# Kernel optimization log

Measured on AMD Instinct MI355X. Metric: run time of the kernel, lower is better.

The kernel has to match this reference:

```python
import jax, jax.numpy as jnp
import numpy as np

B, S, D_IN = 4, 2048, 1024
EMBED, HEADS = 1024, 16
HEAD_DIM = EMBED // HEADS


def setup_inputs() -> dict:
    key = jax.random.key(0)
    k1, k2, k3 = jax.random.split(key, 3)
    x = jax.random.normal(k1, (B, S, D_IN), dtype=jnp.float32)
    # xavier-uniform-ish init scales
    lim_qkv = float(np.sqrt(6.0 / (D_IN + 3 * EMBED)))
    lim_o = float(np.sqrt(6.0 / (EMBED + EMBED)))
    w_qkv = jax.random.uniform(k2, (3 * EMBED, D_IN), minval=-lim_qkv, maxval=lim_qkv, dtype=jnp.float32)
    b_qkv = jnp.zeros((3 * EMBED,), dtype=jnp.float32)
    w_o = jax.random.uniform(k3, (EMBED, EMBED), minval=-lim_o, maxval=lim_o, dtype=jnp.float32)
    b_o = jnp.zeros((EMBED,), dtype=jnp.float32)
    return {"x": x, "w_qkv": w_qkv, "b_qkv": b_qkv, "w_o": w_o, "b_o": b_o}


def reference(x, w_qkv, b_qkv, w_o, b_o):
    b, s, _ = x.shape
    qkv = jnp.einsum('bsi,oi->bso', x, w_qkv) + b_qkv            # (b, s, 3E)
    qkv = qkv.reshape(b, s, HEADS, 3 * HEAD_DIM).transpose(0, 2, 1, 3)  # (b, h, s, 3d)
    q, k, v = jnp.split(qkv, 3, axis=-1)                          # each (b, h, s, d)
    scale = 1.0 / jnp.sqrt(jnp.float32(HEAD_DIM))
    attn = jnp.einsum('bhqd,bhkd->bhqk', q, k) * scale            # (b, h, s, s)
    attn = jax.nn.softmax(attn, axis=-1)
    vals = jnp.einsum('bhqk,bhkd->bhqd', attn, v)                 # (b, h, s, d)
    # NOTE: original torch code reshapes (b,h,s,d) -> (b,s,e) WITHOUT transposing
    # heads back; jnp.reshape reproduces that flattening exactly.
    vals = vals.reshape(b, s, EMBED)
    out = jnp.einsum('bse,oe->bso', vals, w_o) + b_o              # (b, s, E)
    return out
```

## Files before the change

### kernel.cpp

```cpp
#include <hip/hip_runtime.h>
#include <stdint.h>
#include <stddef.h>

#define DEVINL __device__ __forceinline__

typedef unsigned short u16;
typedef unsigned int u32;
typedef __attribute__((ext_vector_type(8))) short short8;
typedef __attribute__((ext_vector_type(4))) float f32x4;
typedef __attribute__((ext_vector_type(4))) u32 u32x4;
typedef __attribute__((ext_vector_type(2))) u32 u32x2;

#define QSCALE 0.18033688011112042f

DEVINL u16 f2bf(float f) {
    u32 u = __builtin_bit_cast(u32, f);
    u32 r = (u + 0x7fffu + ((u >> 16) & 1u)) >> 16;
    return (u16)r;
}

DEVINL void gld_lds16(const void* g, void* l) {
    __builtin_amdgcn_global_load_lds(
        (__attribute__((address_space(1))) u32*)(uintptr_t)g,
        (__attribute__((address_space(3))) u32*)l, 16, 0, 0);
}

DEVINL u32 pack_bf16_trunc(float lo, float hi) {
    return __builtin_amdgcn_perm(__builtin_bit_cast(u32, hi),
                                 __builtin_bit_cast(u32, lo), 0x07060302u);
}

DEVINL void plswap32(u32 &a, u32 &b) {
#if __has_builtin(__builtin_amdgcn_permlane32_swap)
    u32x2 r = __builtin_amdgcn_permlane32_swap(a, b, false, false);
    a = r[0]; b = r[1];
#else
    asm("v_permlane32_swap_b32 %0, %1" : "+v"(a), "+v"(b));
#endif
}
DEVINL void plswap16(u32 &a, u32 &b) {
#if __has_builtin(__builtin_amdgcn_permlane16_swap)
    u32x2 r = __builtin_amdgcn_permlane16_swap(a, b, false, false);
    a = r[0]; b = r[1];
#else
    asm("v_permlane16_swap_b32 %0, %1" : "+v"(a), "+v"(b));
#endif
}

__global__ void prep_inputs(const float* __restrict__ x, const float* __restrict__ wqkv,
                            const float* __restrict__ bqkv, const float* __restrict__ wo,
                            u16* __restrict__ xb, u16* __restrict__ wqb,
                            u16* __restrict__ wob, float* __restrict__ bsc) {
    int blk = blockIdx.x;
    if (blk < 6144) {
        const float* src; u16* dst; int base; bool qscale = false;
        if (blk < 4096)      { src = x;    dst = xb;  base = blk; }
        else if (blk < 5632) { src = wqkv; dst = wqb; base = blk - 4096; qscale = true; }
        else                 { src = wo;   dst = wob; base = blk - 5632; }
        int i = (base * 256 + threadIdx.x) * 8;
        float sc = 1.0f;
        if (qscale) { int row = i >> 10; if ((row % 192) < 64) sc = QSCALE; }
        float4 a = *(const float4*)(src + i);
        float4 c = *(const float4*)(src + i + 4);
        union { u16 s[8]; u32x4 v; } t;
        t.s[0] = f2bf(a.x * sc); t.s[1] = f2bf(a.y * sc); t.s[2] = f2bf(a.z * sc); t.s[3] = f2bf(a.w * sc);
        t.s[4] = f2bf(c.x * sc); t.s[5] = f2bf(c.y * sc); t.s[6] = f2bf(c.z * sc); t.s[7] = f2bf(c.w * sc);
        *(u32x4*)(dst + i) = t.v;
    } else {
        int i = (blk - 6144) * 256 + threadIdx.x;
        float sc = ((i % 192) < 64) ? QSCALE : 1.0f;
        bsc[i] = bqkv[i] * sc;
    }
}

__global__ void gemm_qkv(const u16* __restrict__ A, const u16* __restrict__ Bm,
                         const float* __restrict__ bias, u16* __restrict__ qkvb,
                         u16* __restrict__ vtb) {
    const int K = 1024, N = 3072;
    __shared__ u16 As[128 * 32];
    __shared__ u16 Bs[128 * 32];
    const int tid = threadIdx.x;
    const int lane = tid & 63;
    const int wv = tid >> 6, wr = wv >> 1, wc = wv & 1;
    const int l15 = lane & 15, quad = lane >> 4;
    const int m0 = blockIdx.y * 128, n0 = blockIdx.x * 128;

    f32x4 acc[4][4];
#pragma unroll
    for (int i = 0; i < 4; i++)
#pragma unroll
        for (int j = 0; j < 4; j++) acc[i][j] = (f32x4){0.f, 0.f, 0.f, 0.f};

    const u16* Ab = A + (size_t)m0 * K;
    const u16* Bb = Bm + (size_t)n0 * K;
    const int srow = tid >> 2;
    const int sc8 = (tid & 3) * 8;

    for (int k0 = 0; k0 < K; k0 += 32) {
#pragma unroll
        for (int i = 0; i < 2; i++) {
            int row = i * 64 + srow;
            gld_lds16(Ab + (size_t)row * K + k0 + sc8, (char*)As + (size_t)(i * 256 + tid) * 16);
            gld_lds16(Bb + (size_t)row * K + k0 + sc8, (char*)Bs + (size_t)(i * 256 + tid) * 16);
        }
        __syncthreads();
        short8 af[4], bf8[4];
#pragma unroll
        for (int mi = 0; mi < 4; mi++)
            af[mi] = *(const short8*)(As + (wr * 64 + mi * 16 + l15) * 32 + quad * 8);
#pragma unroll
        for (int ni = 0; ni < 4; ni++)
            bf8[ni] = *(const short8*)(Bs + (wc * 64 + ni * 16 + l15) * 32 + quad * 8);
#pragma unroll
        for (int mi = 0; mi < 4; mi++)
#pragma unroll
            for (int ni = 0; ni < 4; ni++)
                acc[mi][ni] = __builtin_amdgcn_mfma_f32_16x16x32_bf16(af[mi], bf8[ni], acc[mi][ni], 0, 0, 0);
        __syncthreads();
    }

#pragma unroll
    for (int mi = 0; mi < 4; mi++) {
        int row_b = m0 + wr * 64 + mi * 16 + quad * 4;
#pragma unroll
        for (int ni = 0; ni < 4; ni++) {
            int c0 = n0 + wc * 64 + ni * 16;
            int sec0 = c0 % 192;
            float bv = bias[c0 + l15];
            float v0 = acc[mi][ni][0] + bv;
            float v1 = acc[mi][ni][1] + bv;
            float v2 = acc[mi][ni][2] + bv;
            float v3 = acc[mi][ni][3] + bv;
            if (sec0 >= 128) {
                int hh = c0 / 192;
                int b = row_b >> 11;
                int s = row_b & 2047;
                int d = sec0 - 128 + l15;
                u32 lo = (u32)f2bf(v0) | ((u32)f2bf(v1) << 16);
                u32 hi = (u32)f2bf(v2) | ((u32)f2bf(v3) << 16);
                *(u32x2*)(vtb + ((size_t)((b * 16 + hh) * 64 + d)) * 2048 + s) = (u32x2){lo, hi};
            } else {
                int col = c0 + l15;
                qkvb[(size_t)(row_b + 0) * N + col] = f2bf(v0);
                qkvb[(size_t)(row_b + 1) * N + col] = f2bf(v1);
                qkvb[(size_t)(row_b + 2) * N + col] = f2bf(v2);
                qkvb[(size_t)(row_b + 3) * N + col] = f2bf(v3);
            }
        }
    }
}

__global__ void gemm_out(const u16* __restrict__ A, const u16* __restrict__ Bm,
                         const float* __restrict__ bias, float* __restrict__ C) {
    const int K = 1024, N = 1024;
    __shared__ u16 As[128 * 32];
    __shared__ u16 Bs[64 * 32];
    const int tid = threadIdx.x;
    const int lane = tid & 63;
    const int wv = tid >> 6, wr = wv >> 1, wc = wv & 1;
    const int l15 = lane & 15, quad = lane >> 4;
    const int m0 = blockIdx.y * 128, n0 = blockIdx.x * 64;

    f32x4 acc[4][2];
#pragma unroll
    for (int i = 0; i < 4; i++)
#pragma unroll
        for (int j = 0; j < 2; j++) acc[i][j] = (f32x4){0.f, 0.f, 0.f, 0.f};

    const u16* Ab = A + (size_t)m0 * K;
    const u16* Bb = Bm + (size_t)n0 * K;
    const int srow = tid >> 2;
    const int sc8 = (tid & 3) * 8;

    for (int k0 = 0; k0 < K; k0 += 32) {
#pragma unroll
        for (int i = 0; i < 2; i++)
            gld_lds16(Ab + (size_t)(i * 64 + srow) * K + k0 + sc8, (char*)As + (size_t)(i * 256 + tid) * 16);
        gld_lds16(Bb + (size_t)srow * K + k0 + sc8, (char*)Bs + (size_t)tid * 16);
        __syncthreads();
        short8 af[4], bf8[2];
#pragma unroll
        for (int mi = 0; mi < 4; mi++)
            af[mi] = *(const short8*)(As + (wr * 64 + mi * 16 + l15) * 32 + quad * 8);
#pragma unroll
        for (int ni = 0; ni < 2; ni++)
            bf8[ni] = *(const short8*)(Bs + (wc * 32 + ni * 16 + l15) * 32 + quad * 8);
#pragma unroll
        for (int mi = 0; mi < 4; mi++)
#pragma unroll
            for (int ni = 0; ni < 2; ni++)
                acc[mi][ni] = __builtin_amdgcn_mfma_f32_16x16x32_bf16(af[mi], bf8[ni], acc[mi][ni], 0, 0, 0);
        __syncthreads();
    }

#pragma unroll
    for (int mi = 0; mi < 4; mi++) {
        int row_b = m0 + wr * 64 + mi * 16 + quad * 4;
#pragma unroll
        for (int ni = 0; ni < 2; ni++) {
            int col = n0 + wc * 32 + ni * 16 + l15;
            float bv = bias[col];
#pragma unroll
            for (int r = 0; r < 4; r++)
                C[(size_t)(row_b + r) * N + col] = acc[mi][ni][r] + bv;
        }
    }
}

__launch_bounds__(256, 4)
__global__ void flash_attn(const u16* __restrict__ qkv, const u16* __restrict__ vt,
                           u16* __restrict__ vals2) {
    __shared__ u16 Ks[2][64 * 64];
    __shared__ u16 Vts[2][64 * 64];

    const int tid = threadIdx.x;
    const int lane = tid & 63, wv = tid >> 6;
    const int l15 = lane & 15, quad = lane >> 4;
    const int e7 = (l15 & 7) * 8;
    const int s0 = blockIdx.x * 128;
    const int bh = blockIdx.y, b = bh >> 4, h = bh & 15;

    short8 qf[2][2];
    const u16* qbase = qkv + (size_t)(b * 2048 + s0 + wv * 32) * 3072 + h * 192;
#pragma unroll
    for (int qi = 0; qi < 2; qi++)
#pragma unroll
        for (int ks = 0; ks < 2; ks++)
            qf[qi][ks] = *(const short8*)(qbase + (size_t)(qi * 16 + l15) * 3072 + ks * 32 + quad * 8);

    f32x4 o_acc[2][4];
    f32x4 sum_acc[2];
#pragma unroll
    for (int qi = 0; qi < 2; qi++) {
        sum_acc[qi] = (f32x4){0.f, 0.f, 0.f, 0.f};
#pragma unroll
        for (int nd = 0; nd < 4; nd++) o_acc[qi][nd] = (f32x4){0.f, 0.f, 0.f, 0.f};
    }

    const u16* kg = qkv + (size_t)(b * 2048) * 3072 + h * 192 + 64;
    const u16* vg = vt + (size_t)bh * 64 * 2048;

    const int lrow = lane >> 3;
    const int lgr  = (lane & 7) ^ lrow;
    const int r0   = wv * 8 + lrow;

    const short8 ones = (short8){0x3F80, 0x3F80, 0x3F80, 0x3F80, 0x3F80, 0x3F80, 0x3F80, 0x3F80};

#pragma unroll
    for (int j = 0; j < 2; j++) {
        int row = j * 32 + r0;
        gld_lds16(kg + (size_t)row * 3072 + lgr * 8, (char*)&Ks[0][0] + (size_t)(j * 256 + tid) * 16);
        gld_lds16(vg + (size_t)row * 2048 + lgr * 8, (char*)&Vts[0][0] + (size_t)(j * 256 + tid) * 16);
    }
    __syncthreads();

    int cur = 0;
    for (int kb = 0; kb < 2048; kb += 64) {
        if (kb + 64 < 2048) {
            int nb = cur ^ 1;
#pragma unroll
            for (int j = 0; j < 2; j++) {
                int row = j * 32 + r0;
                gld_lds16(kg + (size_t)(kb + 64 + row) * 3072 + lgr * 8,
                          (char*)&Ks[nb][0] + (size_t)(j * 256 + tid) * 16);
                gld_lds16(vg + (size_t)row * 2048 + kb + 64 + lgr * 8,
                          (char*)&Vts[nb][0] + (size_t)(j * 256 + tid) * 16);
            }
        }

        f32x4 s_acc[4][2];
#pragma unroll
        for (int ki = 0; ki < 4; ki++)
#pragma unroll
            for (int qi = 0; qi < 2; qi++) s_acc[ki][qi] = (f32x4){0.f, 0.f, 0.f, 0.f};
#pragma unroll
        for (int ki = 0; ki < 4; ki++) {
#pragma unroll
            for (int ks = 0; ks < 2; ks++) {
                short8 kf = *(const short8*)(&Ks[cur][0] + (ki * 16 + l15) * 64 + ((ks * 32 + quad * 8) ^ e7));
#pragma unroll
                for (int qi = 0; qi < 2; qi++)
                    s_acc[ki][qi] = __builtin_amdgcn_mfma_f32_16x16x32_bf16(kf, qf[qi][ks], s_acc[ki][qi], 0, 0, 0);
            }
        }

        short8 ap[2][2];
#pragma unroll
        for (int c = 0; c < 2; c++)
#pragma unroll
            for (int qi = 0; qi < 2; qi++) {
                u32 w0 = pack_bf16_trunc(__builtin_amdgcn_exp2f(s_acc[2 * c][qi][0]),
                                         __builtin_amdgcn_exp2f(s_acc[2 * c][qi][1]));
                u32 w1 = pack_bf16_trunc(__builtin_amdgcn_exp2f(s_acc[2 * c][qi][2]),
                                         __builtin_amdgcn_exp2f(s_acc[2 * c][qi][3]));
                u32 w2 = pack_bf16_trunc(__builtin_amdgcn_exp2f(s_acc[2 * c + 1][qi][0]),
                                         __builtin_amdgcn_exp2f(s_acc[2 * c + 1][qi][1]));
                u32 w3 = pack_bf16_trunc(__builtin_amdgcn_exp2f(s_acc[2 * c + 1][qi][2]),
                                         __builtin_amdgcn_exp2f(s_acc[2 * c + 1][qi][3]));
                plswap32(w0, w2);
                plswap32(w1, w3);
                plswap16(w0, w2);
                plswap16(w1, w3);
                u32x4 wf = (u32x4){w0, w1, w2, w3};
                ap[qi][c] = __builtin_bit_cast(short8, wf);
            }

#pragma unroll
        for (int c = 0; c < 2; c++) {
#pragma unroll
            for (int qi = 0; qi < 2; qi++)
                sum_acc[qi] = __builtin_amdgcn_mfma_f32_16x16x32_bf16(ap[qi][c], ones, sum_acc[qi], 0, 0, 0);
#pragma unroll
            for (int nd = 0; nd < 4; nd++) {
                short8 bv = *(const short8*)(&Vts[cur][0] + (nd * 16 + l15) * 64 + ((c * 32 + quad * 8) ^ e7));
#pragma unroll
                for (int qi = 0; qi < 2; qi++)
                    o_acc[qi][nd] = __builtin_amdgcn_mfma_f32_16x16x32_bf16(ap[qi][c], bv, o_acc[qi][nd], 0, 0, 0);
            }
        }

        __syncthreads();
        cur ^= 1;
    }

#pragma unroll
    for (int qi = 0; qi < 2; qi++) {
        f32x4 inv;
#pragma unroll
        for (int r = 0; r < 4; r++) inv[r] = 1.0f / sum_acc[qi][r];
#pragma unroll
        for (int nd = 0; nd < 4; nd++) {
            int d = nd * 16 + l15;
#pragma unroll
            for (int r = 0; r < 4; r++) {
                int s = s0 + wv * 32 + qi * 16 + quad * 4 + r;
                size_t row2 = (size_t)(b * 2048 + h * 128 + (s >> 4));
                int col2 = ((s & 15) << 6) + d;
                vals2[row2 * 1024 + col2] = f2bf(o_acc[qi][nd][r] * inv[r]);
            }
        }
    }
}

extern "C" void kernel_launch(void* const* d_in, const int* in_sizes, int n_in,
                              void* d_out, int out_size, void* d_ws, size_t ws_size,
                              hipStream_t stream) {
    (void)in_sizes; (void)n_in; (void)out_size; (void)ws_size;
    const float* x      = (const float*)d_in[0];
    const float* w_qkv  = (const float*)d_in[1];
    const float* b_qkv  = (const float*)d_in[2];
    const float* w_o    = (const float*)d_in[3];
    const float* b_o    = (const float*)d_in[4];
    float* out = (float*)d_out;

    char* ws = (char*)d_ws;
    u16* xb   = (u16*)(ws);
    u16* wqb  = (u16*)(ws + 16777216);
    u16* wob  = (u16*)(ws + 23068672);
    u16* qkvb = (u16*)(ws + 25165824);
    u16* vtb  = (u16*)(ws + 75497472);
    u16* v2b  = (u16*)(ws + 92274688);
    float* bsc = (float*)(ws + 92274688);

    prep_inputs<<<6156, 256, 0, stream>>>(x, w_qkv, b_qkv, w_o, xb, wqb, wob, bsc);

    gemm_qkv<<<dim3(24, 64), 256, 0, stream>>>(xb, wqb, bsc, qkvb, vtb);

    flash_attn<<<dim3(16, 64), 256, 0, stream>>>(qkvb, vtb, v2b);

    gemm_out<<<dim3(16, 64), 256, 0, stream>>>(v2b, wob, b_o, out);
}
```

Measured before the change: 272.2 us.

## Switch flash attention inner loop to 32x32x16 MFMA tiles with priority hints

Rewrites the flash attention inner loop to use 32x32x16 bf16 MFMA instructions instead of 16x16x32, so each wave handles its 32 query rows as a single tile. Q fragments, S scores, the row-sum accumulator and the output accumulator are reorganised around the 32x32 layout. This needs only one permlane32 swap per P fragment instead of 32+16 swaps and cuts the number of MFMA issues and LDS fragment loads. It also adds s_setprio around the MFMA bursts to favour matrix-core issue. The larger accumulators raise register pressure, which may affect occupancy under launch bounds of 4.

```diff
diff --git a/kernel.cpp b/kernel.cpp
--- a/kernel.cpp
+++ b/kernel.cpp
@@ -8,6 +8,7 @@
 typedef unsigned int u32;
 typedef __attribute__((ext_vector_type(8))) short short8;
 typedef __attribute__((ext_vector_type(4))) float f32x4;
+typedef __attribute__((ext_vector_type(16))) float f32x16;
 typedef __attribute__((ext_vector_type(4))) u32 u32x4;
 typedef __attribute__((ext_vector_type(2))) u32 u32x2;
 
@@ -36,14 +37,6 @@
     a = r[0]; b = r[1];
 #else
     asm("v_permlane32_swap_b32 %0, %1" : "+v"(a), "+v"(b));
-#endif
-}
-DEVINL void plswap16(u32 &a, u32 &b) {
-#if __has_builtin(__builtin_amdgcn_permlane16_swap)
-    u32x2 r = __builtin_amdgcn_permlane16_swap(a, b, false, false);
-    a = r[0]; b = r[1];
-#else
-    asm("v_permlane16_swap_b32 %0, %1" : "+v"(a), "+v"(b));
 #endif
 }
 
@@ -215,27 +208,23 @@
 
     const int tid = threadIdx.x;
     const int lane = tid & 63, wv = tid >> 6;
-    const int l15 = lane & 15, quad = lane >> 4;
-    const int e7 = (l15 & 7) * 8;
+    const int l31 = lane & 31, hf = lane >> 5;
+    const int ex = (lane & 7) * 8;
     const int s0 = blockIdx.x * 128;
     const int bh = blockIdx.y, b = bh >> 4, h = bh & 15;
 
-    short8 qf[2][2];
-    const u16* qbase = qkv + (size_t)(b * 2048 + s0 + wv * 32) * 3072 + h * 192;
-#pragma unroll
-    for (int qi = 0; qi < 2; qi++)
-#pragma unroll
-        for (int ks = 0; ks < 2; ks++)
-            qf[qi][ks] = *(const short8*)(qbase + (size_t)(qi * 16 + l15) * 3072 + ks * 32 + quad * 8);
-
-    f32x4 o_acc[2][4];
-    f32x4 sum_acc[2];
-#pragma unroll
-    for (int qi = 0; qi < 2; qi++) {
-        sum_acc[qi] = (f32x4){0.f, 0.f, 0.f, 0.f};
-#pragma unroll
-        for (int nd = 0; nd < 4; nd++) o_acc[qi][nd] = (f32x4){0.f, 0.f, 0.f, 0.f};
-    }
+    short8 qr[4];
+    {
+        const u16* qbase = qkv + (size_t)(b * 2048 + s0 + wv * 32 + l31) * 3072 + h * 192 + hf * 8;
+#pragma unroll
+        for (int ds = 0; ds < 4; ds++)
+            qr[ds] = *(const short8*)(qbase + ds * 16);
+    }
+
+    f32x16 o32[2];
+    f32x16 sum32;
+#pragma unroll
+    for (int i = 0; i < 16; i++) { o32[0][i] = 0.f; o32[1][i] = 0.f; sum32[i] = 0.f; }
 
     const u16* kg = qkv + (size_t)(b * 2048) * 3072 + h * 192 + 64;
     const u16* vg = vt + (size_t)bh * 64 * 2048;
@@ -268,76 +257,63 @@
             }
         }
 
-        f32x4 s_acc[4][2];
-#pragma unroll
-        for (int ki = 0; ki < 4; ki++)
-#pragma unroll
-            for (int qi = 0; qi < 2; qi++) s_acc[ki][qi] = (f32x4){0.f, 0.f, 0.f, 0.f};
-#pragma unroll
-        for (int ki = 0; ki < 4; ki++) {
-#pragma unroll
-            for (int ks = 0; ks < 2; ks++) {
-                short8 kf = *(const short8*)(&Ks[cur][0] + (ki * 16 + l15) * 64 + ((ks * 32 + quad * 8) ^ e7));
-#pragma unroll
-                for (int qi = 0; qi < 2; qi++)
-                    s_acc[ki][qi] = __builtin_amdgcn_mfma_f32_16x16x32_bf16(kf, qf[qi][ks], s_acc[ki][qi], 0, 0, 0);
+#pragma unroll
+        for (int kblk = 0; kblk < 2; kblk++) {
+            f32x16 s32;
+#pragma unroll
+            for (int i = 0; i < 16; i++) s32[i] = 0.f;
+            __builtin_amdgcn_s_setprio(1);
+#pragma unroll
+            for (int ds = 0; ds < 4; ds++) {
+                short8 kf = *(const short8*)(&Ks[cur][0] + (kblk * 32 + l31) * 64 + ((ds * 16 + hf * 8) ^ ex));
+                s32 = __builtin_amdgcn_mfma_f32_32x32x16_bf16(kf, qr[ds], s32, 0, 0, 0);
             }
-        }
-
-        short8 ap[2][2];
-#pragma unroll
-        for (int c = 0; c < 2; c++)
-#pragma unroll
-            for (int qi = 0; qi < 2; qi++) {
-                u32 w0 = pack_bf16_trunc(__builtin_amdgcn_exp2f(s_acc[2 * c][qi][0]),
-                                         __builtin_amdgcn_exp2f(s_acc[2 * c][qi][1]));
-                u32 w1 = pack_bf16_trunc(__builtin_amdgcn_exp2f(s_acc[2 * c][qi][2]),
-                                         __builtin_amdgcn_exp2f(s_acc[2 * c][qi][3]));
-                u32 w2 = pack_bf16_trunc(__builtin_amdgcn_exp2f(s_acc[2 * c + 1][qi][0]),
-                                         __builtin_amdgcn_exp2f(s_acc[2 * c + 1][qi][1]));
-                u32 w3 = pack_bf16_trunc(__builtin_amdgcn_exp2f(s_acc[2 * c + 1][qi][2]),
-                                         __builtin_amdgcn_exp2f(s_acc[2 * c + 1][qi][3]));
-                plswap32(w0, w2);
-                plswap32(w1, w3);
-                plswap16(w0, w2);
-                plswap16(w1, w3);
-                u32x4 wf = (u32x4){w0, w1, w2, w3};
-                ap[qi][c] = __builtin_bit_cast(short8, wf);
+            __builtin_amdgcn_s_setprio(0);
+
+            u32 pw[8];
+#pragma unroll
+            for (int j = 0; j < 8; j++)
+                pw[j] = pack_bf16_trunc(__builtin_amdgcn_exp2f(s32[2 * j]),
+                                        __builtin_amdgcn_exp2f(s32[2 * j + 1]));
+
+#pragma unroll
+            for (int th = 0; th < 2; th++) {
+                const int t = 2 * kblk + th;
+                const int J0 = 4 * th;
+                u32 a0 = pw[J0],     a1 = pw[J0 + 2];
+                u32 b0 = pw[J0 + 1], b1 = pw[J0 + 3];
+                plswap32(a0, a1);
+                plswap32(b0, b1);
+                u32x4 wf = (u32x4){a0, b0, a1, b1};
+                short8 pa = __builtin_bit_cast(short8, wf);
+
+                sum32 = __builtin_amdgcn_mfma_f32_32x32x16_bf16(pa, ones, sum32, 0, 0, 0);
+                __builtin_amdgcn_s_setprio(1);
+#pragma unroll
+                for (int db = 0; db < 2; db++) {
+                    short8 vf = *(const short8*)(&Vts[cur][0] + (db * 32 + l31) * 64 + ((t * 16 + hf * 8) ^ ex));
+                    o32[db] = __builtin_amdgcn_mfma_f32_32x32x16_bf16(pa, vf, o32[db], 0, 0, 0);
+                }
+                __builtin_amdgcn_s_setprio(0);
             }
-
-#pragma unroll
-        for (int c = 0; c < 2; c++) {
-#pragma unroll
-            for (int qi = 0; qi < 2; qi++)
-                sum_acc[qi] = __builtin_amdgcn_mfma_f32_16x16x32_bf16(ap[qi][c], ones, sum_acc[qi], 0, 0, 0);
-#pragma unroll
-            for (int nd = 0; nd < 4; nd++) {
-                short8 bv = *(const short8*)(&Vts[cur][0] + (nd * 16 + l15) * 64 + ((c * 32 + quad * 8) ^ e7));
-#pragma unroll
-                for (int qi = 0; qi < 2; qi++)
-                    o_acc[qi][nd] = __builtin_amdgcn_mfma_f32_16x16x32_bf16(ap[qi][c], bv, o_acc[qi][nd], 0, 0, 0);
-            }
         }
 
         __syncthreads();
         cur ^= 1;
     }
 
-#pragma unroll
-    for (int qi = 0; qi < 2; qi++) {
-        f32x4 inv;
-#pragma unroll
-        for (int r = 0; r < 4; r++) inv[r] = 1.0f / sum_acc[qi][r];
-#pragma unroll
-        for (int nd = 0; nd < 4; nd++) {
-            int d = nd * 16 + l15;
-#pragma unroll
-            for (int r = 0; r < 4; r++) {
-                int s = s0 + wv * 32 + qi * 16 + quad * 4 + r;
-                size_t row2 = (size_t)(b * 2048 + h * 128 + (s >> 4));
-                int col2 = ((s & 15) << 6) + d;
-                vals2[row2 * 1024 + col2] = f2bf(o_acc[qi][nd][r] * inv[r]);
-            }
+    f32x16 inv;
+#pragma unroll
+    for (int r = 0; r < 16; r++) inv[r] = 1.0f / sum32[r];
+#pragma unroll
+    for (int db = 0; db < 2; db++) {
+        int d = db * 32 + l31;
+#pragma unroll
+        for (int r = 0; r < 16; r++) {
+            int s = s0 + wv * 32 + (r & 3) + 8 * (r >> 2) + 4 * hf;
+            size_t row2 = (size_t)(b * 2048 + h * 128 + (s >> 4));
+            int col2 = ((s & 15) << 6) + d;
+            vals2[row2 * 1024 + col2] = f2bf(o32[db][r] * inv[r]);
         }
     }
 }
```

Result: slower. 283.8 us (+4.3%).
